# Kernel tuning notes

Hardware: AMD Instinct MI355X
Metric: run time of the kernel (lower is better)

The kernel has to match this reference:

```python
import jax, jax.numpy as jnp
import numpy as np

DIM, DEPTH, HEADS = 1024, 6, 16
B, N = 2, 1024
QB = 128.0   # 8-bit activation absmax quant: Qb = 2**(8-1)
EPS = 1e-5


def setup_inputs() -> dict:
    key = jax.random.key(0)
    ks = jax.random.split(key, 4)
    x = jax.random.normal(ks[0], (B, N, DIM), dtype=jnp.float32)
    # BitLinear weights (per layer, two per FFN block), latent fp weights
    ff_w1 = jax.random.normal(ks[1], (DEPTH, DIM, DIM), dtype=jnp.float32) * 0.02
    ff_w2 = jax.random.normal(ks[2], (DEPTH, DIM, DIM), dtype=jnp.float32) * 0.02
    # LayerNorm params (inside FeedForward) and final norm
    ff_ln_g = jnp.ones((DEPTH, DIM), jnp.float32)
    ff_ln_b = jnp.zeros((DEPTH, DIM), jnp.float32)
    final_ln_g = jnp.ones((DIM,), jnp.float32)
    final_ln_b = jnp.zeros((DIM,), jnp.float32)
    return dict(x=x, ff_ln_g=ff_ln_g, ff_ln_b=ff_ln_b, ff_w1=ff_w1,
                ff_w2=ff_w2, final_ln_g=final_ln_g, final_ln_b=final_ln_b)


def layernorm(x, g, b):
    m = jnp.mean(x, axis=-1, keepdims=True)
    v = jnp.mean((x - m) ** 2, axis=-1, keepdims=True)
    return (x - m) * jax.lax.rsqrt(v + EPS) * g + b


def bitlinear(x, w):
    # BitNet b1: binarize weights around their mean, absmax-quantize activations to 8 bits,
    # int-style matmul, then rescale by beta*gamma/Qb.
    alpha = jnp.mean(w)
    w_b = jnp.sign(w - alpha)                 # ternary/binary weights {-1,0,+1}
    beta = jnp.mean(jnp.abs(w))               # ||W||_1 / (n*m)
    gamma = jnp.max(jnp.abs(x))               # activation absmax
    x_q = jnp.clip(x * (QB / gamma), -QB + EPS, QB - EPS)
    y = jnp.einsum('...i,oi->...o', x_q, w_b)
    return y * (beta * gamma / QB)


def attend(x):
    # non-flash multi-head self-attention, q=k=v=x (Attend has no projections)
    b, n, d = x.shape
    dh = d // HEADS
    q = x.reshape(b, n, HEADS, dh).transpose(0, 2, 1, 3)          # bhnd
    scores = jnp.einsum('bhid,bhjd->bhij', q, q) * (dh ** -0.5)   # [B,H,N,N]
    attn = jax.nn.softmax(scores, axis=-1)
    out = jnp.einsum('bhij,bhjd->bhid', attn, q)
    return out.transpose(0, 2, 1, 3).reshape(b, n, d)


def reference(x, ff_ln_g, ff_ln_b, ff_w1, ff_w2, final_ln_g, final_ln_b):
    for i in range(DEPTH):
        x = attend(x) + x
        h = layernorm(x, ff_ln_g[i], ff_ln_b[i])
        h = bitlinear(h, ff_w1[i])
        h = jax.nn.gelu(h, approximate=False)   # torch nn.GELU default = exact
        h = bitlinear(h, ff_w2[i])
        x = h + x
    return layernorm(x, final_ln_g, final_ln_b)
```

## Files before the change

### kernel.cpp

```cpp
#include <hip/hip_runtime.h>
#include <math.h>

typedef __attribute__((ext_vector_type(4))) float f32x4;
typedef __attribute__((ext_vector_type(8))) _Float16 f16x8;

__device__ __forceinline__ f32x4 mfma16h(f16x8 a, f16x8 b, f32x4 c){
  return __builtin_amdgcn_mfma_f32_16x16x32_f16(a, b, c, 0, 0, 0);
}
__device__ __forceinline__ void gload_lds16(const void* g, void* l){
  __builtin_amdgcn_global_load_lds((const __attribute__((address_space(1))) void*)g,
                                   (__attribute__((address_space(3))) void*)l, 16, 0, 0);
}

#define EXPC 0.1803368801111204f
#define PHI(n) (((((n)>>3)&1)<<2) | ((((n)>>1)&1)<<1) | ((n)&1))

__global__ __launch_bounds__(256) void k_wstats(const float* __restrict__ w1, const float* __restrict__ w2,
                                                double* __restrict__ dsum, double* __restrict__ dabs){
  const int mat = blockIdx.y;
  const float* wp = (mat < 6) ? (w1 + (size_t)mat*1048576) : (w2 + (size_t)(mat-6)*1048576);
  const f32x4* wv = (const f32x4*)wp + (size_t)blockIdx.x*8192;
  double s = 0.0, a = 0.0;
  for (int j = 0; j < 32; j++){
    f32x4 v = wv[j*256 + threadIdx.x];
    s += (double)v.x + (double)v.y + (double)v.z + (double)v.w;
    a += (double)fabsf(v.x) + (double)fabsf(v.y) + (double)fabsf(v.z) + (double)fabsf(v.w);
  }
  for (int d = 1; d < 64; d <<= 1){ s += __shfl_xor(s, d); a += __shfl_xor(a, d); }
  __shared__ double red[8];
  const int w = threadIdx.x >> 6;
  if ((threadIdx.x & 63) == 0){ red[w*2] = s; red[w*2+1] = a; }
  __syncthreads();
  if (threadIdx.x == 0){
    double S = red[0]+red[2]+red[4]+red[6], A = red[1]+red[3]+red[5]+red[7];
    atomicAdd(&dsum[mat], S);
    atomicAdd(&dabs[mat], A);
  }
}

__global__ __launch_bounds__(256) void k_binarize(const float* __restrict__ w1, const float* __restrict__ w2,
                                                  const double* __restrict__ dsum, _Float16* __restrict__ wb){
  const int blk = blockIdx.x;
  const int mat = blk >> 9;
  const float alpha = (float)(dsum[mat] * (1.0/1048576.0));
  const float* wp = (mat < 6) ? (w1 + (size_t)mat*1048576) : (w2 + (size_t)(mat-6)*1048576);
  const size_t off = (size_t)(blk & 511)*2048 + (size_t)threadIdx.x*8;
  const int n = (int)(off >> 10), k = (int)(off & 1023);
  f32x4 v0 = *(const f32x4*)(wp + off), v1 = *(const f32x4*)(wp + off + 4);
  float vv[8] = {v0.x,v0.y,v0.z,v0.w,v1.x,v1.y,v1.z,v1.w};
  f16x8 pk;
  #pragma unroll
  for (int e = 0; e < 8; e++){
    float d = vv[e] - alpha;
    pk[e] = d > 0.f ? (_Float16)1.0f : (d < 0.f ? (_Float16)(-1.0f) : (_Float16)0.0f);
  }
  const size_t addr = (size_t)mat*1048576 + (size_t)n*1024 + (size_t)((k & ~63) + ((k & 63) ^ ((n&7)*8)));
  *(f16x8*)&wb[addr] = pk;
}

__global__ __launch_bounds__(256) void k_presplit(const float* __restrict__ x,
                                                  _Float16* __restrict__ Kh, _Float16* __restrict__ Kl,
                                                  _Float16* __restrict__ Vh, _Float16* __restrict__ Vl){
  __shared__ _Float16 lh[64*72], ll[64*72];
  const int t = blockIdx.x, bh = blockIdx.y, b = bh>>4, h = bh&15;
  const int n = threadIdx.x>>2, c0 = (threadIdx.x&3)*16;
  const float* src = x + (size_t)b*1048576 + (size_t)(t*64+n)*1024 + h*64 + c0;
  const size_t kbase = ((size_t)bh*1024 + t*64 + n)*64;
  const int sw = PHI(n)*8;
  #pragma unroll
  for (int j = 0; j < 2; j++){
    f32x4 v0 = *(const f32x4*)(src + j*8);
    f32x4 v1 = *(const f32x4*)(src + j*8 + 4);
    float vv[8] = {v0.x,v0.y,v0.z,v0.w,v1.x,v1.y,v1.z,v1.w};
    f16x8 Hv, Lv;
    #pragma unroll
    for (int e = 0; e < 8; e++){
      _Float16 hh = (_Float16)vv[e];
      Hv[e] = hh; Lv[e] = (_Float16)(vv[e] - (float)hh);
      const int d = c0 + j*8 + e;
      lh[d*72 + n] = Hv[e]; ll[d*72 + n] = Lv[e];
    }
    const int db = c0 + j*8;
    *(f16x8*)&Kh[kbase + (db ^ sw)] = Hv;
    *(f16x8*)&Kl[kbase + (db ^ sw)] = Lv;
  }
  __syncthreads();
  const int d = threadIdx.x>>2, n0c = (threadIdx.x&3)*16;
  const size_t vbase = ((size_t)bh*64 + d)*1024 + t*64;
  const int sw2 = (d&7)*8;
  #pragma unroll
  for (int j = 0; j < 2; j++){
    const int nb = n0c + j*8;
    *(f16x8*)&Vh[vbase + (nb ^ sw2)] = *(const f16x8*)&lh[d*72 + nb];
    *(f16x8*)&Vl[vbase + (nb ^ sw2)] = *(const f16x8*)&ll[d*72 + nb];
  }
}

__global__ __launch_bounds__(256) void k_attn(const _Float16* __restrict__ Kh, const _Float16* __restrict__ Kl,
                                              const _Float16* __restrict__ Vh, const _Float16* __restrict__ Vl,
                                              const float* __restrict__ xin, float* __restrict__ xout){
  __shared__ _Float16 smb[40960];
  _Float16* qs_h = smb + 32768;
  _Float16* qs_l = smb + 36864;
  const int tid = threadIdx.x, w = tid>>6, l = tid&63, g = l>>4, r16 = l&15;
  const int bh = blockIdx.x, qt = blockIdx.y, b = bh>>4, h = bh&15;
  const _Float16* Kbh = Kh + (size_t)bh*65536;
  const _Float16* Kbl = Kl + (size_t)bh*65536;

  size_t koffK[2], voff[2];
  int cbj[2];
  #pragma unroll
  for (int j = 0; j < 2; j++){
    const int cb = (j*4 + w)*64, c = cb + l;
    const int p  = c>>3;
    const int kp = (p&32) | ((p&12)<<1) | ((p&16)>>2) | (p&3);
    cbj[j]   = cb;
    koffK[j] = (size_t)kp*64 + (size_t)(l&7)*8;
    voff[j]  = ((size_t)bh*64 + (c>>3))*1024 + (size_t)(c&7)*8;
  }
  #define ASTAGE(buf, t) { _Float16* Bp = smb + (buf)*16384;                         \
    _Pragma("unroll")                                                                 \
    for (int j = 0; j < 2; j++){                                                      \
      gload_lds16(Kbh + (size_t)(t)*4096 + koffK[j], Bp + cbj[j]*8);                  \
      gload_lds16(Kbl + (size_t)(t)*4096 + koffK[j], Bp + 4096 + cbj[j]*8);           \
      gload_lds16(Vh + voff[j] + (t)*64, Bp + 8192 + cbj[j]*8);                       \
      gload_lds16(Vl + voff[j] + (t)*64, Bp + 12288 + cbj[j]*8);                      \
    } }

  const _Float16* Qsh = Kbh + (size_t)qt*4096;
  const _Float16* Qsl = Kbl + (size_t)qt*4096;
  #pragma unroll
  for (int j = 0; j < 2; j++){
    const int cb = cbj[j];
    gload_lds16(Qsh + (size_t)(cb + l)*8, qs_h + cb*8);
    gload_lds16(Qsl + (size_t)(cb + l)*8, qs_l + cb*8);
  }
  ASTAGE(0, 0);
  __syncthreads();
  const int qrow = w*16 + r16;
  const int phq8 = PHI(qrow)*8;
  const int swk8 = (r16&7)*8;
  const int swr8 = (r16&7)*8;
  const f16x8 aqh0 = *(const f16x8*)&qs_h[qrow*64 + ((g*8) ^ phq8)];
  const f16x8 aqh1 = *(const f16x8*)&qs_h[qrow*64 + ((32 + g*8) ^ phq8)];
  const f16x8 aql0 = *(const f16x8*)&qs_l[qrow*64 + ((g*8) ^ phq8)];
  const f16x8 aql1 = *(const f16x8*)&qs_l[qrow*64 + ((32 + g*8) ^ phq8)];
  float mI = -1e30f, lI = 0.f;
  f32x4 acc[4];
  #pragma unroll
  for (int i = 0; i < 4; i++) acc[i] = (f32x4){0.f,0.f,0.f,0.f};

  for (int t = 0; t < 16; t++){
    if (t < 15) ASTAGE((t+1)&1, t+1);
    const _Float16* kt_h = smb + (t&1)*16384;
    const _Float16* kt_l = kt_h + 4096;
    const _Float16* vt_h = kt_h + 8192;
    const _Float16* vt_l = kt_h + 12288;
    f32x4 s[4];
    #pragma unroll
    for (int c = 0; c < 4; c++){
      const int rk = c*16 + r16;
      const f16x8 kh0 = *(const f16x8*)&kt_h[rk*64 + ((g*8) ^ swk8)];
      const f16x8 kh1 = *(const f16x8*)&kt_h[rk*64 + ((32+g*8) ^ swk8)];
      const f16x8 kl0 = *(const f16x8*)&kt_l[rk*64 + ((g*8) ^ swk8)];
      const f16x8 kl1 = *(const f16x8*)&kt_l[rk*64 + ((32+g*8) ^ swk8)];
      f32x4 z = (f32x4){0.f,0.f,0.f,0.f};
      z = mfma16h(kh0, aqh0, z);
      z = mfma16h(kh1, aqh1, z);
      z = mfma16h(kh0, aql0, z);
      z = mfma16h(kh1, aql1, z);
      z = mfma16h(kl0, aqh0, z);
      z = mfma16h(kl1, aqh1, z);
      s[c] = z;
    }
    float rmax = s[0][0];
    #pragma unroll
    for (int c = 0; c < 4; c++)
      #pragma unroll
      for (int i = 0; i < 4; i++) rmax = fmaxf(rmax, s[c][i]);
    rmax = fmaxf(rmax, __shfl_xor(rmax, 16));
    rmax = fmaxf(rmax, __shfl_xor(rmax, 32));
    if (__any(rmax - mI > 44.36f)){
      const float mn = fmaxf(mI, rmax);
      const float fac = exp2f((mI - mn)*EXPC);
      lI *= fac;
      mI = mn;
      #pragma unroll
      for (int i = 0; i < 4; i++){
        const float fi = __shfl(fac, g*4 + i);
        #pragma unroll
        for (int dc = 0; dc < 4; dc++) acc[dc][i] *= fi;
      }
    }
    const float mC = mI*EXPC;
    float rsum = 0.f;
    f16x8 aph[2], apl[2];
    #pragma unroll
    for (int c = 0; c < 4; c++)
      #pragma unroll
      for (int i = 0; i < 4; i++){
        const float p = exp2f(fmaf(s[c][i], EXPC, -mC));
        const _Float16 ph = (_Float16)p;
        aph[c>>1][(c&1)*4 + i] = ph;
        apl[c>>1][(c&1)*4 + i] = (_Float16)(p - (float)ph);
        rsum += p;
      }
    rsum += __shfl_xor(rsum, 16);
    rsum += __shfl_xor(rsum, 32);
    lI += rsum;
    #pragma unroll
    for (int ks = 0; ks < 2; ks++){
      #pragma unroll
      for (int dc = 0; dc < 4; dc++){
        const int vr = dc*16 + r16;
        const f16x8 bvh = *(const f16x8*)&vt_h[vr*64 + ((ks*32 + g*8) ^ swr8)];
        const f16x8 bvl = *(const f16x8*)&vt_l[vr*64 + ((ks*32 + g*8) ^ swr8)];
        acc[dc] = mfma16h(aph[ks], bvh, acc[dc]);
        acc[dc] = mfma16h(apl[ks], bvh, acc[dc]);
        acc[dc] = mfma16h(aph[ks], bvl, acc[dc]);
      }
    }
    __syncthreads();
  }
  #undef ASTAGE
  #pragma unroll
  for (int i = 0; i < 4; i++){
    const float li = __shfl(lI, g*4 + i);
    const float inv = 1.f/li;
    const int row = qt*64 + w*16 + g*4 + i;
    #pragma unroll
    for (int dc = 0; dc < 4; dc++){
      const size_t idx = (size_t)b*1048576 + (size_t)row*1024 + h*64 + dc*16 + r16;
      xout[idx] = acc[dc][i]*inv + xin[idx];
    }
  }
}

template<int SPLIT>
__global__ __launch_bounds__(256) void k_ln(const float* __restrict__ x, const float* __restrict__ gg,
                                            const float* __restrict__ bb, float* __restrict__ outf,
                                            _Float16* __restrict__ Oh, _Float16* __restrict__ Ol){
  const int row = blockIdx.x*4 + (threadIdx.x>>6);
  const int lane = threadIdx.x & 63;
  const float* xr = x + (size_t)row*1024;
  f32x4 v[4];
  float s = 0.f, q = 0.f;
  #pragma unroll
  for (int c = 0; c < 2; c++){
    v[c*2]   = *(const f32x4*)(xr + c*512 + lane*8);
    v[c*2+1] = *(const f32x4*)(xr + c*512 + lane*8 + 4);
    #pragma unroll
    for (int e = 0; e < 4; e++){
      s += v[c*2][e] + v[c*2+1][e];
      q += v[c*2][e]*v[c*2][e] + v[c*2+1][e]*v[c*2+1][e];
    }
  }
  for (int d = 1; d < 64; d <<= 1){ s += __shfl_xor(s,d); q += __shfl_xor(q,d); }
  const float mean = s * (1.f/1024.f);
  const float var  = q * (1.f/1024.f) - mean*mean;
  const float rstd = rsqrtf(var + 1e-5f);
  #pragma unroll
  for (int c = 0; c < 2; c++){
    const int col = c*512 + lane*8;
    f32x4 g0 = *(const f32x4*)(gg + col), g1 = *(const f32x4*)(gg + col + 4);
    f32x4 b0 = *(const f32x4*)(bb + col), b1 = *(const f32x4*)(bb + col + 4);
    float h[8];
    #pragma unroll
    for (int e = 0; e < 4; e++){
      h[e]   = (v[c*2][e]  -mean)*rstd*g0[e] + b0[e];
      h[e+4] = (v[c*2+1][e]-mean)*rstd*g1[e] + b1[e];
    }
    if (SPLIT){
      f16x8 Hv, Lv;
      #pragma unroll
      for (int e = 0; e < 8; e++){
        _Float16 hh = (_Float16)h[e];
        Hv[e] = hh; Lv[e] = (_Float16)(h[e] - (float)hh);
      }
      const size_t addr = (size_t)row*1024 + c*512 + (lane>>3)*64 + (((lane&7)*8) ^ ((row&7)*8));
      *(f16x8*)&Oh[addr] = Hv;
      *(f16x8*)&Ol[addr] = Lv;
    } else {
      f32x4 o0, o1;
      #pragma unroll
      for (int e = 0; e < 4; e++){ o0[e] = h[e]; o1[e] = h[e+4]; }
      *(f32x4*)(outf + (size_t)row*1024 + col) = o0;
      *(f32x4*)(outf + (size_t)row*1024 + col + 4) = o1;
    }
  }
}

template<int MODE>
__global__ __launch_bounds__(256) void k_gemm(const _Float16* __restrict__ Ah, const _Float16* __restrict__ Al,
                                              const _Float16* __restrict__ Wg,
                                              float* __restrict__ out32,
                                              _Float16* __restrict__ Oh, _Float16* __restrict__ Ol,
                                              const double* __restrict__ dabs_slot,
                                              _Float16* __restrict__ Kh, _Float16* __restrict__ Kl,
                                              _Float16* __restrict__ Vh, _Float16* __restrict__ Vl){
  __shared__ _Float16 smb[24576];
  const int tid = threadIdx.x, w = tid>>6, l = tid&63, g = l>>4, r16 = l&15;
  const int wm = w>>1, wn = w&1;
  const int n0 = blockIdx.x*64, m0 = blockIdx.y*64;
  const float scale = (float)(*dabs_slot * (1.0/1048576.0));
  const int swr = (r16&7)*8;
  f32x4 acc[2][2] = {};
  #define STAGE(buf, k0) { _Float16* Bp = smb + (buf)*12288;                              \
    _Pragma("unroll")                                                                     \
    for (int j = 0; j < 2; j++){                                                          \
      const int cb = (j*4 + w)*64; const int c = cb + l;                                  \
      const int r = c>>3; const int cc = (c&7)*8;                                         \
      gload_lds16(Ah + (size_t)(m0 + r)*1024 + (k0) + cc, Bp + cb*8);                     \
      gload_lds16(Al + (size_t)(m0 + r)*1024 + (k0) + cc, Bp + 4096 + cb*8);              \
      gload_lds16(Wg + (size_t)(n0 + r)*1024 + (k0) + cc, Bp + 8192 + cb*8);              \
    } }
  STAGE(0, 0);
  __syncthreads();
  for (int t = 0; t < 16; t++){
    if (t < 15) STAGE((t+1)&1, (t+1)*64);
    const _Float16* Bp = smb + (t&1)*12288;
    #pragma unroll
    for (int kk = 0; kk < 2; kk++){
      f16x8 ah[2], al[2], bf[2];
      const int col = (kk*32 + g*8) ^ swr;
      #pragma unroll
      for (int mi = 0; mi < 2; mi++){
        const int row = wm*32 + mi*16 + r16;
        ah[mi] = *(const f16x8*)&Bp[row*64 + col];
        al[mi] = *(const f16x8*)&Bp[4096 + row*64 + col];
      }
      #pragma unroll
      for (int ni = 0; ni < 2; ni++){
        const int row = wn*32 + ni*16 + r16;
        bf[ni] = *(const f16x8*)&Bp[8192 + row*64 + col];
      }
      #pragma unroll
      for (int mi = 0; mi < 2; mi++)
        #pragma unroll
        for (int ni = 0; ni < 2; ni++){
          acc[mi][ni] = mfma16h(ah[mi], bf[ni], acc[mi][ni]);
          acc[mi][ni] = mfma16h(al[mi], bf[ni], acc[mi][ni]);
        }
    }
    __syncthreads();
  }
  #undef STAGE
  _Float16* kh_t = smb;
  _Float16* kl_t = smb + 4608;
  _Float16* lhv  = smb + 9216;
  _Float16* llv  = smb + 13824;
  #pragma unroll
  for (int mi = 0; mi < 2; mi++)
    #pragma unroll
    for (int ni = 0; ni < 2; ni++)
      #pragma unroll
      for (int i = 0; i < 4; i++){
        const int rr = m0 + wm*32 + mi*16 + g*4 + i;
        const int cc = n0 + wn*32 + ni*16 + r16;
        float vv = acc[mi][ni][i] * scale;
        if (MODE == 0){
          vv = 0.5f*vv*(1.f + erff(vv*0.70710678118f));
          _Float16 hh = (_Float16)vv;
          const size_t addr = (size_t)rr*1024 + (cc & ~63) + ((cc & 63) ^ ((rr&7)*8));
          Oh[addr] = hh;
          Ol[addr] = (_Float16)(vv - (float)hh);
        } else {
          const size_t idx = (size_t)rr*1024 + cc;
          const float xnew = out32[idx] + vv;
          out32[idx] = xnew;
          if (Kh){
            const int nl = wm*32 + mi*16 + g*4 + i;
            const int dl = wn*32 + ni*16 + r16;
            const _Float16 hh = (_Float16)xnew;
            const _Float16 lo = (_Float16)(xnew - (float)hh);
            kh_t[nl*72 + dl] = hh;  kl_t[nl*72 + dl] = lo;
            lhv [dl*72 + nl] = hh;  llv [dl*72 + nl] = lo;
          }
        }
      }
  if (MODE == 1 && Kh){
    __syncthreads();
    const int n = tid>>2, c0q = (tid&3)*16;
    const int bh = (blockIdx.y>>4)*16 + blockIdx.x;
    const int tseq = blockIdx.y & 15;
    const size_t kbase = ((size_t)bh*1024 + tseq*64 + n)*64;
    const int swn = PHI(n)*8;
    const size_t vbase = ((size_t)bh*64 + n)*1024 + tseq*64;
    const int sw2 = (n&7)*8;
    #pragma unroll
    for (int j = 0; j < 2; j++){
      const int db = c0q + j*8;
      *(f16x8*)&Kh[kbase + (db ^ swn)] = *(const f16x8*)&kh_t[n*72 + db];
      *(f16x8*)&Kl[kbase + (db ^ swn)] = *(const f16x8*)&kl_t[n*72 + db];
      *(f16x8*)&Vh[vbase + (db ^ sw2)] = *(const f16x8*)&lhv[n*72 + db];
      *(f16x8*)&Vl[vbase + (db ^ sw2)] = *(const f16x8*)&llv[n*72 + db];
    }
  }
}

extern "C" void kernel_launch(void* const* d_in, const int* in_sizes, int n_in,
                              void* d_out, int out_size, void* d_ws, size_t ws_size,
                              hipStream_t stream){
  const float* x_in = (const float*)d_in[0];
  const float* ln_g = (const float*)d_in[1];
  const float* ln_b = (const float*)d_in[2];
  const float* w1   = (const float*)d_in[3];
  const float* w2   = (const float*)d_in[4];
  const float* fg   = (const float*)d_in[5];
  const float* fb   = (const float*)d_in[6];

  char* ws = (char*)d_ws;
  double*   dsum  = (double*)ws;
  double*   dabs  = (double*)(ws + 96);
  _Float16* wb = (_Float16*)(ws + 256);
  size_t o = 256 + 12ull*1048576ull*2ull;
  float* xA = (float*)(ws + o); o += 2048ull*1024*4;
  float* xB = (float*)(ws + o); o += 2048ull*1024*4;
  _Float16* Kh = (_Float16*)(ws + o); o += 2048ull*1024*2;
  _Float16* Kl = (_Float16*)(ws + o); o += 2048ull*1024*2;
  _Float16* Vh = (_Float16*)(ws + o); o += 2048ull*1024*2;
  _Float16* Vl = (_Float16*)(ws + o); o += 2048ull*1024*2;
  _Float16* Ahb = (_Float16*)(ws + o); o += 2048ull*1024*2;
  _Float16* Alb = (_Float16*)(ws + o); o += 2048ull*1024*2;
  _Float16* Ghb = (_Float16*)(ws + o); o += 2048ull*1024*2;
  _Float16* Glb = (_Float16*)(ws + o); o += 2048ull*1024*2;

  hipMemsetAsync(ws, 0, 256, stream);
  k_wstats  <<<dim3(32,12), 256, 0, stream>>>(w1, w2, dsum, dabs);
  k_binarize<<<6144,        256, 0, stream>>>(w1, w2, dsum, wb);
  k_presplit<<<dim3(16,32), 256, 0, stream>>>(x_in, Kh, Kl, Vh, Vl);

  const float* xc = x_in;
  for (int i = 0; i < 6; i++){
    float* xn = (i & 1) ? xB : xA;
    const bool last = (i == 5);
    k_attn    <<<dim3(32,16), 256, 0, stream>>>(Kh, Kl, Vh, Vl, xc, xn);
    k_ln<1>   <<<512, 256, 0, stream>>>(xn, ln_g + (size_t)i*1024, ln_b + (size_t)i*1024,
                                        nullptr, Ahb, Alb);
    k_gemm<0> <<<dim3(16,32), 256, 0, stream>>>(Ahb, Alb, wb + (size_t)i*1048576,
                                                nullptr, Ghb, Glb, &dabs[i],
                                                nullptr, nullptr, nullptr, nullptr);
    k_gemm<1> <<<dim3(16,32), 256, 0, stream>>>(Ghb, Glb, wb + (size_t)(6+i)*1048576,
                                                xn, nullptr, nullptr, &dabs[6+i],
                                                last ? nullptr : Kh, last ? nullptr : Kl,
                                                last ? nullptr : Vh, last ? nullptr : Vl);
    xc = xn;
  }
  k_ln<0><<<512, 256, 0, stream>>>(xc, fg, fb, (float*)d_out, nullptr, nullptr);
}
```

Before: 512.8 us.

## Process 128 query rows per attention block to reuse K/V tiles

```diff
diff --git a/kernel.cpp b/kernel.cpp
--- a/kernel.cpp
+++ b/kernel.cpp
@@ -96,12 +96,10 @@
   }
 }
 
-__global__ __launch_bounds__(256) void k_attn(const _Float16* __restrict__ Kh, const _Float16* __restrict__ Kl,
-                                              const _Float16* __restrict__ Vh, const _Float16* __restrict__ Vl,
-                                              const float* __restrict__ xin, float* __restrict__ xout){
-  __shared__ _Float16 smb[40960];
-  _Float16* qs_h = smb + 32768;
-  _Float16* qs_l = smb + 36864;
+__global__ __launch_bounds__(256, 1) void k_attn(const _Float16* __restrict__ Kh, const _Float16* __restrict__ Kl,
+                                                 const _Float16* __restrict__ Vh, const _Float16* __restrict__ Vl,
+                                                 const float* __restrict__ xin, float* __restrict__ xout){
+  __shared__ _Float16 smb[32768];
   const int tid = threadIdx.x, w = tid>>6, l = tid&63, g = l>>4, r16 = l&15;
   const int bh = blockIdx.x, qt = blockIdx.y, b = bh>>4, h = bh&15;
   const _Float16* Kbh = Kh + (size_t)bh*65536;
@@ -127,28 +125,38 @@
       gload_lds16(Vl + voff[j] + (t)*64, Bp + 12288 + cbj[j]*8);                      \
     } }
 
-  const _Float16* Qsh = Kbh + (size_t)qt*4096;
-  const _Float16* Qsl = Kbl + (size_t)qt*4096;
-  #pragma unroll
-  for (int j = 0; j < 2; j++){
-    const int cb = cbj[j];
+  const _Float16* Qsh = Kbh + (size_t)qt*8192;
+  const _Float16* Qsl = Kbl + (size_t)qt*8192;
+  _Float16* qs_h = smb;
+  _Float16* qs_l = smb + 8192;
+  #pragma unroll
+  for (int j = 0; j < 4; j++){
+    const int cb = (j*4 + w)*64;
     gload_lds16(Qsh + (size_t)(cb + l)*8, qs_h + cb*8);
     gload_lds16(Qsl + (size_t)(cb + l)*8, qs_l + cb*8);
   }
+  __syncthreads();
+  f16x8 aqh[2][2], aql[2][2];
+  #pragma unroll
+  for (int s2 = 0; s2 < 2; s2++){
+    const int qrl = w*32 + s2*16 + r16;
+    const int phq8 = PHI(qrl & 63)*8;
+    aqh[s2][0] = *(const f16x8*)&qs_h[qrl*64 + ((g*8) ^ phq8)];
+    aqh[s2][1] = *(const f16x8*)&qs_h[qrl*64 + ((32 + g*8) ^ phq8)];
+    aql[s2][0] = *(const f16x8*)&qs_l[qrl*64 + ((g*8) ^ phq8)];
+    aql[s2][1] = *(const f16x8*)&qs_l[qrl*64 + ((32 + g*8) ^ phq8)];
+  }
+  __syncthreads();
   ASTAGE(0, 0);
   __syncthreads();
-  const int qrow = w*16 + r16;
-  const int phq8 = PHI(qrow)*8;
+
   const int swk8 = (r16&7)*8;
-  const int swr8 = (r16&7)*8;
-  const f16x8 aqh0 = *(const f16x8*)&qs_h[qrow*64 + ((g*8) ^ phq8)];
-  const f16x8 aqh1 = *(const f16x8*)&qs_h[qrow*64 + ((32 + g*8) ^ phq8)];
-  const f16x8 aql0 = *(const f16x8*)&qs_l[qrow*64 + ((g*8) ^ phq8)];
-  const f16x8 aql1 = *(const f16x8*)&qs_l[qrow*64 + ((32 + g*8) ^ phq8)];
-  float mI = -1e30f, lI = 0.f;
-  f32x4 acc[4];
-  #pragma unroll
-  for (int i = 0; i < 4; i++) acc[i] = (f32x4){0.f,0.f,0.f,0.f};
+  float mI[2] = {-1e30f, -1e30f}, lI[2] = {0.f, 0.f};
+  f32x4 acc[2][4];
+  #pragma unroll
+  for (int s2 = 0; s2 < 2; s2++)
+    #pragma unroll
+    for (int i = 0; i < 4; i++) acc[s2][i] = (f32x4){0.f,0.f,0.f,0.f};
 
   for (int t = 0; t < 16; t++){
     if (t < 15) ASTAGE((t+1)&1, t+1);
@@ -156,7 +164,7 @@
     const _Float16* kt_l = kt_h + 4096;
     const _Float16* vt_h = kt_h + 8192;
     const _Float16* vt_l = kt_h + 12288;
-    f32x4 s[4];
+    f32x4 s[2][4];
     #pragma unroll
     for (int c = 0; c < 4; c++){
       const int rk = c*16 + r16;
@@ -164,76 +172,95 @@
       const f16x8 kh1 = *(const f16x8*)&kt_h[rk*64 + ((32+g*8) ^ swk8)];
       const f16x8 kl0 = *(const f16x8*)&kt_l[rk*64 + ((g*8) ^ swk8)];
       const f16x8 kl1 = *(const f16x8*)&kt_l[rk*64 + ((32+g*8) ^ swk8)];
-      f32x4 z = (f32x4){0.f,0.f,0.f,0.f};
-      z = mfma16h(kh0, aqh0, z);
-      z = mfma16h(kh1, aqh1, z);
-      z = mfma16h(kh0, aql0, z);
-      z = mfma16h(kh1, aql1, z);
-      z = mfma16h(kl0, aqh0, z);
-      z = mfma16h(kl1, aqh1, z);
-      s[c] = z;
-    }
-    float rmax = s[0][0];
-    #pragma unroll
-    for (int c = 0; c < 4; c++)
-      #pragma unroll
-      for (int i = 0; i < 4; i++) rmax = fmaxf(rmax, s[c][i]);
-    rmax = fmaxf(rmax, __shfl_xor(rmax, 16));
-    rmax = fmaxf(rmax, __shfl_xor(rmax, 32));
-    if (__any(rmax - mI > 44.36f)){
-      const float mn = fmaxf(mI, rmax);
-      const float fac = exp2f((mI - mn)*EXPC);
-      lI *= fac;
-      mI = mn;
-      #pragma unroll
-      for (int i = 0; i < 4; i++){
-        const float fi = __shfl(fac, g*4 + i);
+      #pragma unroll
+      for (int s2 = 0; s2 < 2; s2++){
+        f32x4 z = (f32x4){0.f,0.f,0.f,0.f};
+        z = mfma16h(kh0, aqh[s2][0], z);
+        z = mfma16h(kh1, aqh[s2][1], z);
+        z = mfma16h(kh0, aql[s2][0], z);
+        z = mfma16h(kh1, aql[s2][1], z);
+        z = mfma16h(kl0, aqh[s2][0], z);
+        z = mfma16h(kl1, aqh[s2][1], z);
+        s[s2][c] = z;
+      }
+    }
+    float rmax[2];
+    #pragma unroll
+    for (int s2 = 0; s2 < 2; s2++){
+      float rm = s[s2][0][0];
+      #pragma unroll
+      for (int c = 0; c < 4; c++)
         #pragma unroll
-        for (int dc = 0; dc < 4; dc++) acc[dc][i] *= fi;
-      }
-    }
-    const float mC = mI*EXPC;
-    float rsum = 0.f;
-    f16x8 aph[2], apl[2];
-    #pragma unroll
-    for (int c = 0; c < 4; c++)
-      #pragma unroll
-      for (int i = 0; i < 4; i++){
-        const float p = exp2f(fmaf(s[c][i], EXPC, -mC));
-        const _Float16 ph = (_Float16)p;
-        aph[c>>1][(c&1)*4 + i] = ph;
-        apl[c>>1][(c&1)*4 + i] = (_Float16)(p - (float)ph);
-        rsum += p;
-      }
-    rsum += __shfl_xor(rsum, 16);
-    rsum += __shfl_xor(rsum, 32);
-    lI += rsum;
+        for (int i = 0; i < 4; i++) rm = fmaxf(rm, s[s2][c][i]);
+      rm = fmaxf(rm, __shfl_xor(rm, 16));
+      rm = fmaxf(rm, __shfl_xor(rm, 32));
+      rmax[s2] = rm;
+    }
+    if (__any(fmaxf(rmax[0]-mI[0], rmax[1]-mI[1]) > 44.36f)){
+      #pragma unroll
+      for (int s2 = 0; s2 < 2; s2++){
+        const float mn = fmaxf(mI[s2], rmax[s2]);
+        const float fac = exp2f((mI[s2] - mn)*EXPC);
+        lI[s2] *= fac;
+        mI[s2] = mn;
+        #pragma unroll
+        for (int i = 0; i < 4; i++){
+          const float fi = __shfl(fac, g*4 + i);
+          #pragma unroll
+          for (int dc = 0; dc < 4; dc++) acc[s2][dc][i] *= fi;
+        }
+      }
+    }
+    f16x8 aph[2][2], apl[2][2];
+    #pragma unroll
+    for (int s2 = 0; s2 < 2; s2++){
+      const float mC = mI[s2]*EXPC;
+      float rsum = 0.f;
+      #pragma unroll
+      for (int c = 0; c < 4; c++)
+        #pragma unroll
+        for (int i = 0; i < 4; i++){
+          const float p = exp2f(fmaf(s[s2][c][i], EXPC, -mC));
+          const _Float16 ph = (_Float16)p;
+          aph[s2][c>>1][(c&1)*4 + i] = ph;
+          apl[s2][c>>1][(c&1)*4 + i] = (_Float16)(p - (float)ph);
+          rsum += p;
+        }
+      rsum += __shfl_xor(rsum, 16);
+      rsum += __shfl_xor(rsum, 32);
+      lI[s2] += rsum;
+    }
     #pragma unroll
     for (int ks = 0; ks < 2; ks++){
       #pragma unroll
       for (int dc = 0; dc < 4; dc++){
         const int vr = dc*16 + r16;
-        const f16x8 bvh = *(const f16x8*)&vt_h[vr*64 + ((ks*32 + g*8) ^ swr8)];
-        const f16x8 bvl = *(const f16x8*)&vt_l[vr*64 + ((ks*32 + g*8) ^ swr8)];
-        acc[dc] = mfma16h(aph[ks], bvh, acc[dc]);
-        acc[dc] = mfma16h(apl[ks], bvh, acc[dc]);
-        acc[dc] = mfma16h(aph[ks], bvl, acc[dc]);
+        const f16x8 bvh = *(const f16x8*)&vt_h[vr*64 + ((ks*32 + g*8) ^ swk8)];
+        const f16x8 bvl = *(const f16x8*)&vt_l[vr*64 + ((ks*32 + g*8) ^ swk8)];
+        #pragma unroll
+        for (int s2 = 0; s2 < 2; s2++){
+          acc[s2][dc] = mfma16h(aph[s2][ks], bvh, acc[s2][dc]);
+          acc[s2][dc] = mfma16h(apl[s2][ks], bvh, acc[s2][dc]);
+          acc[s2][dc] = mfma16h(aph[s2][ks], bvl, acc[s2][dc]);
+        }
       }
     }
     __syncthreads();
   }
   #undef ASTAGE
   #pragma unroll
-  for (int i = 0; i < 4; i++){
-    const float li = __shfl(lI, g*4 + i);
-    const float inv = 1.f/li;
-    const int row = qt*64 + w*16 + g*4 + i;
-    #pragma unroll
-    for (int dc = 0; dc < 4; dc++){
-      const size_t idx = (size_t)b*1048576 + (size_t)row*1024 + h*64 + dc*16 + r16;
-      xout[idx] = acc[dc][i]*inv + xin[idx];
-    }
-  }
+  for (int s2 = 0; s2 < 2; s2++)
+    #pragma unroll
+    for (int i = 0; i < 4; i++){
+      const float li = __shfl(lI[s2], g*4 + i);
+      const float inv = 1.f/li;
+      const int row = qt*128 + w*32 + s2*16 + g*4 + i;
+      #pragma unroll
+      for (int dc = 0; dc < 4; dc++){
+        const size_t idx = (size_t)b*1048576 + (size_t)row*1024 + h*64 + dc*16 + r16;
+        xout[idx] = acc[s2][dc][i]*inv + xin[idx];
+      }
+    }
 }
 
 template<int SPLIT>
@@ -434,7 +461,7 @@
   for (int i = 0; i < 6; i++){
     float* xn = (i & 1) ? xB : xA;
     const bool last = (i == 5);
-    k_attn    <<<dim3(32,16), 256, 0, stream>>>(Kh, Kl, Vh, Vl, xc, xn);
+    k_attn    <<<dim3(32,8), 256, 0, stream>>>(Kh, Kl, Vh, Vl, xc, xn);
     k_ln<1>   <<<512, 256, 0, stream>>>(xn, ln_g + (size_t)i*1024, ln_b + (size_t)i*1024,
                                         nullptr, Ahb, Alb);
     k_gemm<0> <<<dim3(16,32), 256, 0, stream>>>(Ahb, Alb, wb + (size_t)i*1048576,
```

After: 525.5 us. 1.02x slower.

## Software-pipeline attention: overlap next-tile QK^T with current softmax/PV

Applied to the files above, without the earlier changes.

```diff
diff --git a/kernel.cpp b/kernel.cpp
--- a/kernel.cpp
+++ b/kernel.cpp
@@ -100,8 +100,6 @@
                                               const _Float16* __restrict__ Vh, const _Float16* __restrict__ Vl,
                                               const float* __restrict__ xin, float* __restrict__ xout){
   __shared__ _Float16 smb[40960];
-  _Float16* qs_h = smb + 32768;
-  _Float16* qs_l = smb + 36864;
   const int tid = threadIdx.x, w = tid>>6, l = tid&63, g = l>>4, r16 = l&15;
   const int bh = blockIdx.x, qt = blockIdx.y, b = bh>>4, h = bh&15;
   const _Float16* Kbh = Kh + (size_t)bh*65536;
@@ -118,111 +116,136 @@
     koffK[j] = (size_t)kp*64 + (size_t)(l&7)*8;
     voff[j]  = ((size_t)bh*64 + (c>>3))*1024 + (size_t)(c&7)*8;
   }
-  #define ASTAGE(buf, t) { _Float16* Bp = smb + (buf)*16384;                         \
-    _Pragma("unroll")                                                                 \
+  #define KSTAGE(PK, T) { _Pragma("unroll")                                          \
     for (int j = 0; j < 2; j++){                                                      \
-      gload_lds16(Kbh + (size_t)(t)*4096 + koffK[j], Bp + cbj[j]*8);                  \
-      gload_lds16(Kbl + (size_t)(t)*4096 + koffK[j], Bp + 4096 + cbj[j]*8);           \
-      gload_lds16(Vh + voff[j] + (t)*64, Bp + 8192 + cbj[j]*8);                       \
-      gload_lds16(Vl + voff[j] + (t)*64, Bp + 12288 + cbj[j]*8);                      \
+      gload_lds16(Kbh + (size_t)(T)*4096 + koffK[j], (PK) + cbj[j]*8);                \
+      gload_lds16(Kbl + (size_t)(T)*4096 + koffK[j], (PK) + 4096 + cbj[j]*8);         \
     } }
-
-  const _Float16* Qsh = Kbh + (size_t)qt*4096;
-  const _Float16* Qsl = Kbl + (size_t)qt*4096;
-  #pragma unroll
-  for (int j = 0; j < 2; j++){
-    const int cb = cbj[j];
-    gload_lds16(Qsh + (size_t)(cb + l)*8, qs_h + cb*8);
-    gload_lds16(Qsl + (size_t)(cb + l)*8, qs_l + cb*8);
-  }
-  ASTAGE(0, 0);
-  __syncthreads();
+  #define VSTAGE(PV, T) { _Pragma("unroll")                                          \
+    for (int j = 0; j < 2; j++){                                                      \
+      gload_lds16(Vh + voff[j] + (T)*64, (PV) + cbj[j]*8);                            \
+      gload_lds16(Vl + voff[j] + (T)*64, (PV) + 4096 + cbj[j]*8);                     \
+    } }
+
+  _Float16* pKo = smb;
+  _Float16* pKn = smb + 8192;
+  _Float16* pKs = smb + 16384;
+  _Float16* pVc = smb + 24576;
+  _Float16* pVs = smb + 32768;
+
+  KSTAGE(pKo, 0); KSTAGE(pKn, 1); VSTAGE(pVc, 0);
   const int qrow = w*16 + r16;
   const int phq8 = PHI(qrow)*8;
+  const size_t qb = (size_t)qt*4096 + (size_t)qrow*64;
+  const f16x8 aqh0 = *(const f16x8*)&Kbh[qb + ((g*8) ^ phq8)];
+  const f16x8 aqh1 = *(const f16x8*)&Kbh[qb + ((32 + g*8) ^ phq8)];
+  const f16x8 aql0 = *(const f16x8*)&Kbl[qb + ((g*8) ^ phq8)];
+  const f16x8 aql1 = *(const f16x8*)&Kbl[qb + ((32 + g*8) ^ phq8)];
+  __syncthreads();
+
   const int swk8 = (r16&7)*8;
-  const int swr8 = (r16&7)*8;
-  const f16x8 aqh0 = *(const f16x8*)&qs_h[qrow*64 + ((g*8) ^ phq8)];
-  const f16x8 aqh1 = *(const f16x8*)&qs_h[qrow*64 + ((32 + g*8) ^ phq8)];
-  const f16x8 aql0 = *(const f16x8*)&qs_l[qrow*64 + ((g*8) ^ phq8)];
-  const f16x8 aql1 = *(const f16x8*)&qs_l[qrow*64 + ((32 + g*8) ^ phq8)];
   float mI = -1e30f, lI = 0.f;
-  f32x4 acc[4];
+  f32x4 acc[4], sA[4], sB[4];
   #pragma unroll
   for (int i = 0; i < 4; i++) acc[i] = (f32x4){0.f,0.f,0.f,0.f};
 
-  for (int t = 0; t < 16; t++){
-    if (t < 15) ASTAGE((t+1)&1, t+1);
-    const _Float16* kt_h = smb + (t&1)*16384;
-    const _Float16* kt_l = kt_h + 4096;
-    const _Float16* vt_h = kt_h + 8192;
-    const _Float16* vt_l = kt_h + 12288;
-    f32x4 s[4];
-    #pragma unroll
-    for (int c = 0; c < 4; c++){
-      const int rk = c*16 + r16;
-      const f16x8 kh0 = *(const f16x8*)&kt_h[rk*64 + ((g*8) ^ swk8)];
-      const f16x8 kh1 = *(const f16x8*)&kt_h[rk*64 + ((32+g*8) ^ swk8)];
-      const f16x8 kl0 = *(const f16x8*)&kt_l[rk*64 + ((g*8) ^ swk8)];
-      const f16x8 kl1 = *(const f16x8*)&kt_l[rk*64 + ((32+g*8) ^ swk8)];
-      f32x4 z = (f32x4){0.f,0.f,0.f,0.f};
-      z = mfma16h(kh0, aqh0, z);
-      z = mfma16h(kh1, aqh1, z);
-      z = mfma16h(kh0, aql0, z);
-      z = mfma16h(kh1, aql1, z);
-      z = mfma16h(kl0, aqh0, z);
-      z = mfma16h(kl1, aqh1, z);
-      s[c] = z;
-    }
-    float rmax = s[0][0];
-    #pragma unroll
-    for (int c = 0; c < 4; c++)
-      #pragma unroll
-      for (int i = 0; i < 4; i++) rmax = fmaxf(rmax, s[c][i]);
-    rmax = fmaxf(rmax, __shfl_xor(rmax, 16));
-    rmax = fmaxf(rmax, __shfl_xor(rmax, 32));
-    if (__any(rmax - mI > 44.36f)){
-      const float mn = fmaxf(mI, rmax);
-      const float fac = exp2f((mI - mn)*EXPC);
-      lI *= fac;
-      mI = mn;
-      #pragma unroll
-      for (int i = 0; i < 4; i++){
-        const float fi = __shfl(fac, g*4 + i);
-        #pragma unroll
-        for (int dc = 0; dc < 4; dc++) acc[dc][i] *= fi;
-      }
-    }
-    const float mC = mI*EXPC;
-    float rsum = 0.f;
-    f16x8 aph[2], apl[2];
-    #pragma unroll
-    for (int c = 0; c < 4; c++)
-      #pragma unroll
-      for (int i = 0; i < 4; i++){
-        const float p = exp2f(fmaf(s[c][i], EXPC, -mC));
-        const _Float16 ph = (_Float16)p;
-        aph[c>>1][(c&1)*4 + i] = ph;
-        apl[c>>1][(c&1)*4 + i] = (_Float16)(p - (float)ph);
-        rsum += p;
-      }
-    rsum += __shfl_xor(rsum, 16);
-    rsum += __shfl_xor(rsum, 32);
-    lI += rsum;
-    #pragma unroll
-    for (int ks = 0; ks < 2; ks++){
-      #pragma unroll
-      for (int dc = 0; dc < 4; dc++){
-        const int vr = dc*16 + r16;
-        const f16x8 bvh = *(const f16x8*)&vt_h[vr*64 + ((ks*32 + g*8) ^ swr8)];
-        const f16x8 bvl = *(const f16x8*)&vt_l[vr*64 + ((ks*32 + g*8) ^ swr8)];
-        acc[dc] = mfma16h(aph[ks], bvh, acc[dc]);
-        acc[dc] = mfma16h(apl[ks], bvh, acc[dc]);
-        acc[dc] = mfma16h(aph[ks], bvl, acc[dc]);
-      }
-    }
-    __syncthreads();
-  }
-  #undef ASTAGE
+  #define QKT(PK, SD) { const _Float16* kt_h = (PK); const _Float16* kt_l = (PK) + 4096;  \
+    _Pragma("unroll")                                                                      \
+    for (int c = 0; c < 4; c++){                                                           \
+      const int rk = c*16 + r16;                                                           \
+      const f16x8 kh0 = *(const f16x8*)&kt_h[rk*64 + ((g*8) ^ swk8)];                      \
+      const f16x8 kh1 = *(const f16x8*)&kt_h[rk*64 + ((32+g*8) ^ swk8)];                   \
+      const f16x8 kl0 = *(const f16x8*)&kt_l[rk*64 + ((g*8) ^ swk8)];                      \
+      const f16x8 kl1 = *(const f16x8*)&kt_l[rk*64 + ((32+g*8) ^ swk8)];                   \
+      f32x4 z = (f32x4){0.f,0.f,0.f,0.f};                                                  \
+      z = mfma16h(kh0, aqh0, z);                                                           \
+      z = mfma16h(kh1, aqh1, z);                                                           \
+      z = mfma16h(kh0, aql0, z);                                                           \
+      z = mfma16h(kh1, aql1, z);                                                           \
+      z = mfma16h(kl0, aqh0, z);                                                           \
+      z = mfma16h(kl1, aqh1, z);                                                           \
+      (SD)[c] = z;                                                                         \
+    } }
+
+  #define SMAXPV(SC) {                                                                     \
+    float rmax = (SC)[0][0];                                                               \
+    _Pragma("unroll")                                                                      \
+    for (int c = 0; c < 4; c++)                                                            \
+      _Pragma("unroll")                                                                    \
+      for (int i = 0; i < 4; i++) rmax = fmaxf(rmax, (SC)[c][i]);                          \
+    rmax = fmaxf(rmax, __shfl_xor(rmax, 16));                                              \
+    rmax = fmaxf(rmax, __shfl_xor(rmax, 32));                                              \
+    if (__any(rmax - mI > 44.36f)){                                                        \
+      const float mn = fmaxf(mI, rmax);                                                    \
+      const float fac = exp2f((mI - mn)*EXPC);                                             \
+      lI *= fac;                                                                           \
+      mI = mn;                                                                             \
+      _Pragma("unroll")                                                                    \
+      for (int i = 0; i < 4; i++){                                                         \
+        const float fi = __shfl(fac, g*4 + i);                                             \
+        _Pragma("unroll")                                                                  \
+        for (int dc = 0; dc < 4; dc++) acc[dc][i] *= fi;                                   \
+      }                                                                                    \
+    }                                                                                      \
+    const float mC = mI*EXPC;                                                              \
+    float rsum = 0.f;                                                                      \
+    f16x8 aph[2], apl[2];                                                                  \
+    _Pragma("unroll")                                                                      \
+    for (int c = 0; c < 4; c++)                                                            \
+      _Pragma("unroll")                                                                    \
+      for (int i = 0; i < 4; i++){                                                         \
+        const float p = exp2f(fmaf((SC)[c][i], EXPC, -mC));                                \
+        const _Float16 ph = (_Float16)p;                                                   \
+        aph[c>>1][(c&1)*4 + i] = ph;                                                       \
+        apl[c>>1][(c&1)*4 + i] = (_Float16)(p - (float)ph);                                \
+        rsum += p;                                                                         \
+      }                                                                                    \
+    rsum += __shfl_xor(rsum, 16);                                                          \
+    rsum += __shfl_xor(rsum, 32);                                                          \
+    lI += rsum;                                                                            \
+    const _Float16* vt_h = pVc; const _Float16* vt_l = pVc + 4096;                         \
+    _Pragma("unroll")                                                                      \
+    for (int ks = 0; ks < 2; ks++){                                                        \
+      _Pragma("unroll")                                                                    \
+      for (int dc = 0; dc < 4; dc++){                                                      \
+        const int vr = dc*16 + r16;                                                        \
+        const f16x8 bvh = *(const f16x8*)&vt_h[vr*64 + ((ks*32 + g*8) ^ swk8)];            \
+        const f16x8 bvl = *(const f16x8*)&vt_l[vr*64 + ((ks*32 + g*8) ^ swk8)];            \
+        acc[dc] = mfma16h(aph[ks], bvh, acc[dc]);                                          \
+        acc[dc] = mfma16h(apl[ks], bvh, acc[dc]);                                          \
+        acc[dc] = mfma16h(aph[ks], bvl, acc[dc]);                                          \
+      }                                                                                    \
+    } }
+
+  QKT(pKo, sA);
+
+  for (int tt = 0; tt < 8; tt++){
+    {
+      const int t = 2*tt;
+      if (t < 14) KSTAGE(pKs, t+2);
+      VSTAGE(pVs, t+1);
+      QKT(pKn, sB);
+      SMAXPV(sA);
+      __syncthreads();
+      _Float16* tk = pKo; pKo = pKn; pKn = pKs; pKs = tk;
+      _Float16* tv = pVc; pVc = pVs; pVs = tv;
+    }
+    {
+      const int t = 2*tt+1;
+      if (t < 14) KSTAGE(pKs, t+2);
+      if (t < 15) VSTAGE(pVs, t+1);
+      if (t < 15) QKT(pKn, sA);
+      SMAXPV(sB);
+      __syncthreads();
+      _Float16* tk = pKo; pKo = pKn; pKn = pKs; pKs = tk;
+      _Float16* tv = pVc; pVc = pVs; pVs = tv;
+    }
+  }
+  #undef KSTAGE
+  #undef VSTAGE
+  #undef QKT
+  #undef SMAXPV
+
   #pragma unroll
   for (int i = 0; i < 4; i++){
     const float li = __shfl(lI, g*4 + i);
```

Measured after the change: 509.5 us. No clear change (-0.6%).
